# Performance work log

Measured on AMD Instinct MI355X. Metric: run time of the kernel, lower is better.

## Reference

```python
import jax, jax.numpy as jnp
import numpy as np

N, IN_FEAT, OUT_FEAT = 8192, 512, 256
SLOPE = 0.1


def setup_inputs() -> dict:
    key = jax.random.key(0)
    k1, k2, k3, k4, k5 = jax.random.split(key, 5)
    doc = jax.random.normal(k1, (N, IN_FEAT), dtype=jnp.float32)
    W = jax.random.normal(k2, (IN_FEAT, OUT_FEAT), dtype=jnp.float32) * (1.0 / np.sqrt(IN_FEAT))
    W_b = jax.random.normal(k3, (OUT_FEAT,), dtype=jnp.float32) * 0.01
    a = jax.random.normal(k4, (2 * OUT_FEAT,), dtype=jnp.float32) * (1.0 / np.sqrt(2 * OUT_FEAT))
    a_b = jax.random.normal(k5, (1,), dtype=jnp.float32) * 0.01
    return {"doc": doc, "W": W, "W_b": W_b, "a": a, "a_b": a_b}


def reference(doc, W, W_b, a, a_b):
    # h = W(doc): [N, outFeat]
    h = doc @ W + W_b
    d = h.shape[-1]
    # aParams(cat(h_i, h_j)) = a1.h_i + a2.h_j + b  (avoids the O(N^2*2d) concat)
    a1, a2 = a[:d], a[d:]
    score = (h @ a1)[:, None] + (h @ a2)[None, :] + a_b[0]  # [N, N]
    score = jax.nn.leaky_relu(score, SLOPE)
    # adj=None path -> all-ones mask, the where() is a no-op
    att = jax.nn.softmax(score, axis=1)  # normalize over neighbors j
    out = jax.nn.leaky_relu(att @ h, SLOPE)  # [N, outFeat]
    return out, att
```

## Files before the change

kernel.cpp:

```cpp
#include <hip/hip_runtime.h>
#include <hip/hip_bf16.h>


typedef __attribute__((ext_vector_type(4))) float f32x4;
typedef __attribute__((ext_vector_type(8))) short short8;
typedef __attribute__((ext_vector_type(4))) unsigned short ushort4v;

#define SLOPE 0.1f
#define NROW 8192
#define DDIM 256

__device__ __forceinline__ float lrelu(float x){ return fmaxf(x, SLOPE * x); }

__device__ __forceinline__ unsigned short f2bf(float f){
  union { float f; unsigned u; } v; v.f = f;
  unsigned r = (v.u + 0x7fffu + ((v.u >> 16) & 1u)) >> 16;
  return (unsigned short)r;
}
__device__ __forceinline__ float bf2f(unsigned short u){
  union { unsigned u; float f; } v; v.u = (unsigned)u << 16; return v.f;
}
__device__ __forceinline__ unsigned cvt_pk_bf16(float lo, float hi){
  unsigned r;
  asm("v_cvt_pk_bf16_f32 %0, %1, %2" : "=v"(r) : "v"(lo), "v"(hi));
  return r;
}

__global__ __launch_bounds__(256) void k_prep(
    const float* __restrict__ W,
    unsigned short* __restrict__ Wt_hi, unsigned short* __restrict__ Wt_lo)
{
  const int tid = blockIdx.x * 256 + threadIdx.x;
  const int c = tid >> 7, kq = tid & 127;
  ushort4v hi, lo;
#pragma unroll
  for (int j = 0; j < 4; ++j) {
    const float v = W[(size_t)(kq * 4 + j) * 256 + c];
    hi[j] = f2bf(v);
    lo[j] = f2bf(v - bf2f(hi[j]));
  }
  *reinterpret_cast<ushort4v*>(Wt_hi + (size_t)c * 512 + kq * 4) = hi;
  *reinterpret_cast<ushort4v*>(Wt_lo + (size_t)c * 512 + kq * 4) = lo;
}

__global__ __launch_bounds__(512, 2) void k_h(
    const float* __restrict__ doc, const unsigned short* __restrict__ Wt_hi,
    const unsigned short* __restrict__ Wt_lo, const float* __restrict__ Wb,
    const float* __restrict__ a,
    unsigned short* __restrict__ ht, float* __restrict__ s1,
    float* __restrict__ e2, float* __restrict__ e02)
{
  __shared__ __align__(16) short8 aH[2][2][64];
  __shared__ __align__(16) short8 aL[2][2][64];
  __shared__ float sred[8][2][32];

  const int t = threadIdx.x, w = t >> 6, l = t & 63;
  const int lr = l & 15, lg = l >> 4;
  const int rb = blockIdx.x * 32;
  const int cb = w * 32;

  f32x4 acc[2][2];
#pragma unroll
  for (int rt = 0; rt < 2; ++rt)
#pragma unroll
    for (int ct = 0; ct < 2; ++ct) acc[rt][ct] = (f32x4){0.f, 0.f, 0.f, 0.f};

  const float* docp = doc + (size_t)(rb + w * 16 + lr) * 512 + lg * 8;

  f32x4 v0, v1;
  auto loadDoc = [&](int k0) { if (w < 2) {
      v0 = *reinterpret_cast<const f32x4*>(docp + k0);
      v1 = *reinterpret_cast<const f32x4*>(docp + k0 + 4);
  }};
  auto writeStage = [&](int pb) { if (w < 2) {
      union { short8 v; unsigned short u[8]; } hi, lo;
#pragma unroll
      for (int q = 0; q < 4; ++q) {
        hi.u[q] = f2bf(v0[q]);     lo.u[q] = f2bf(v0[q] - bf2f(hi.u[q]));
        hi.u[4+q] = f2bf(v1[q]);   lo.u[4+q] = f2bf(v1[q] - bf2f(hi.u[4+q]));
      }
      aH[pb][w][l] = hi.v;
      aL[pb][w][l] = lo.v;
  }};

  loadDoc(0); writeStage(0); loadDoc(32);

  for (int n = 0; n < 16; ++n) {
    const int kk = n * 32;
    const int par = n & 1;

    asm volatile("s_waitcnt lgkmcnt(0)\n\ts_barrier" ::: "memory");

    const short8 ah0 = aH[par][0][l];
    const short8 ah1 = aH[par][1][l];
    const short8 al0 = aL[par][0][l];
    const short8 al1 = aL[par][1][l];

    short8 bh[2], bl[2];
#pragma unroll
    for (int ct = 0; ct < 2; ++ct) {
      const size_t off = (size_t)(cb + ct * 16 + lr) * 512 + kk + lg * 8;
      bh[ct] = *reinterpret_cast<const short8*>(Wt_hi + off);
      bl[ct] = *reinterpret_cast<const short8*>(Wt_lo + off);
    }

    if (n + 1 < 16) writeStage(par ^ 1);
    if (n + 2 < 16) loadDoc((n + 2) * 32);

#pragma unroll
    for (int ct = 0; ct < 2; ++ct) {
      acc[0][ct] = __builtin_amdgcn_mfma_f32_16x16x32_bf16(ah0, bh[ct], acc[0][ct], 0, 0, 0);
      acc[1][ct] = __builtin_amdgcn_mfma_f32_16x16x32_bf16(ah1, bh[ct], acc[1][ct], 0, 0, 0);
      acc[0][ct] = __builtin_amdgcn_mfma_f32_16x16x32_bf16(ah0, bl[ct], acc[0][ct], 0, 0, 0);
      acc[1][ct] = __builtin_amdgcn_mfma_f32_16x16x32_bf16(ah1, bl[ct], acc[1][ct], 0, 0, 0);
      acc[0][ct] = __builtin_amdgcn_mfma_f32_16x16x32_bf16(al0, bh[ct], acc[0][ct], 0, 0, 0);
      acc[1][ct] = __builtin_amdgcn_mfma_f32_16x16x32_bf16(al1, bh[ct], acc[1][ct], 0, 0, 0);
    }
  }

  float bias[2];
#pragma unroll
  for (int ct = 0; ct < 2; ++ct) bias[ct] = Wb[cb + ct * 16 + lr];
#pragma unroll
  for (int rt = 0; rt < 2; ++rt)
#pragma unroll
    for (int ct = 0; ct < 2; ++ct) {
#pragma unroll
      for (int q = 0; q < 4; ++q) acc[rt][ct][q] += bias[ct];
      ushort4v u;
#pragma unroll
      for (int q = 0; q < 4; ++q) u[q] = f2bf(acc[rt][ct][q]);
      *reinterpret_cast<ushort4v*>(
          ht + (size_t)(cb + ct * 16 + lr) * 8192 + rb + rt * 16 + lg * 4) = u;
    }

  float a1c[2], a2c[2];
#pragma unroll
  for (int ct = 0; ct < 2; ++ct) {
    a1c[ct] = a[cb + ct * 16 + lr];
    a2c[ct] = a[256 + cb + ct * 16 + lr];
  }
  float p1[2][4], p2[2][4];
#pragma unroll
  for (int rt = 0; rt < 2; ++rt)
#pragma unroll
    for (int q = 0; q < 4; ++q) {
      float x1 = 0.f, x2 = 0.f;
#pragma unroll
      for (int ct = 0; ct < 2; ++ct) {
        x1 = fmaf(acc[rt][ct][q], a1c[ct], x1);
        x2 = fmaf(acc[rt][ct][q], a2c[ct], x2);
      }
#pragma unroll
      for (int off = 1; off < 16; off <<= 1) {
        x1 += __shfl_xor(x1, off);
        x2 += __shfl_xor(x2, off);
      }
      p1[rt][q] = x1; p2[rt][q] = x2;
    }
  __syncthreads();
  if (lr == 0) {
#pragma unroll
    for (int rt = 0; rt < 2; ++rt)
#pragma unroll
      for (int q = 0; q < 4; ++q) {
        sred[w][0][rt * 16 + lg * 4 + q] = p1[rt][q];
        sred[w][1][rt * 16 + lg * 4 + q] = p2[rt][q];
      }
  }
  __syncthreads();
  if (t < 32) {
    float v1s = 0.f, v2s = 0.f;
#pragma unroll
    for (int ww = 0; ww < 8; ++ww) { v1s += sred[ww][0][t]; v2s += sred[ww][1][t]; }
    const int r = rb + t;
    s1[r] = v1s;
    e2[r] = __expf(v2s);
    e02[r] = __expf(SLOPE * v2s);
  }
}

__global__ __launch_bounds__(256) void k_z(
    const float* __restrict__ s1, const float* __restrict__ e2g,
    const float* __restrict__ e02g, const float* __restrict__ abp,
    float* __restrict__ rowinfo)
{
  __shared__ __align__(16) float es[8192];
  __shared__ __align__(16) float fs[8192];
  const int t = threadIdx.x;
  for (int i = t * 4; i < 8192; i += 1024) {
    *reinterpret_cast<f32x4*>(&es[i]) = *reinterpret_cast<const f32x4*>(e2g + i);
    *reinterpret_cast<f32x4*>(&fs[i]) = *reinterpret_cast<const f32x4*>(e02g + i);
  }
  __syncthreads();
  const int w = t >> 6, l = t & 63;
  const float ab = abp[0];
  const int rb = blockIdx.x * 16 + w * 4;
  float T[4], E1[4], E01[4];
#pragma unroll
  for (int rr = 0; rr < 4; ++rr) {
    const float s1a = s1[rb + rr] + ab;
    E1[rr] = __expf(s1a); E01[rr] = __expf(SLOPE * s1a); T[rr] = __expf(-s1a);
  }
  float zA[4] = {0.f,0.f,0.f,0.f}, zB[4] = {0.f,0.f,0.f,0.f};
  for (int i = l * 4; i < 8192; i += 256) {
    const f32x4 e = *reinterpret_cast<const f32x4*>(&es[i]);
    const f32x4 f = *reinterpret_cast<const f32x4*>(&fs[i]);
#pragma unroll
    for (int rr = 0; rr < 4; ++rr)
#pragma unroll
      for (int q = 0; q < 4; ++q) {
        const bool c = (e[q] >= T[rr]);
        zA[rr] += c ? e[q] : 0.f;
        zB[rr] += c ? 0.f : f[q];
      }
  }
#pragma unroll
  for (int rr = 0; rr < 4; ++rr) {
    float z = E1[rr] * zA[rr] + E01[rr] * zB[rr];
#pragma unroll
    for (int off = 32; off > 0; off >>= 1) z += __shfl_down(z, off);
    if (l == 0) {
      const float iz = 1.0f / z;
      f32x4 ri = (f32x4){E1[rr] * iz, E01[rr] * iz, T[rr], iz};
      *reinterpret_cast<f32x4*>(rowinfo + (size_t)(rb + rr) * 4) = ri;
    }
  }
}

__global__ __launch_bounds__(512, 4) void k_att(
    const float* __restrict__ rowinfo, const float* __restrict__ e2g,
    const float* __restrict__ e02g, const unsigned short* __restrict__ ht,
    float* __restrict__ att, float* __restrict__ part, int CHUNK)
{
  extern __shared__ __align__(16) char smem[];
  char* plsb  = smem;
  float* e2s  = reinterpret_cast<float*>(smem + 8192);
  float* e02s = e2s + CHUNK;

  const int t = threadIdx.x, w = t >> 6, l = t & 63;
  const int lr = l & 15, lg = l >> 4;
  const int kbase = blockIdx.x * CHUNK;
  const int rb = blockIdx.y * 64;

  for (int i = t * 4; i < CHUNK; i += 2048) {
    *reinterpret_cast<f32x4*>(e2s + i)  = *reinterpret_cast<const f32x4*>(e2g + kbase + i);
    *reinterpret_cast<f32x4*>(e02s + i) = *reinterpret_cast<const f32x4*>(e02g + kbase + i);
  }

  const int r = l >> 3, jc = l & 7;
  const int rowW = rb + w * 8 + r;
  const f32x4 ri = *reinterpret_cast<const f32x4*>(rowinfo + (size_t)rowW * 4);
  const float E1z = ri[0], E01z = ri[1], T = ri[2];
  float* attW = att + (size_t)rowW * 8192 + kbase + jc * 4;
  const int fragoff = (w >> 1) * 1024 + ((jc >> 1) * 16 + (w & 1) * 8 + r) * 16 + (jc & 1) * 8;

  __syncthreads();

  auto gen = [&](int kw, int pb) {
    const f32x4 eA = *reinterpret_cast<const f32x4*>(e2s + kw + jc * 4);
    const f32x4 fA = *reinterpret_cast<const f32x4*>(e02s + kw + jc * 4);
    f32x4 pA;
#pragma unroll
    for (int q = 0; q < 4; ++q) {
      const bool cA = (eA[q] >= T);
      pA[q] = (cA ? E1z : E01z) * (cA ? eA[q] : fA[q]);
    }
    *reinterpret_cast<f32x4*>(attW + kw) = pA;
    uint2 u;
    u.x = cvt_pk_bf16(pA[0], pA[1]); u.y = cvt_pk_bf16(pA[2], pA[3]);
    *reinterpret_cast<uint2*>(plsb + pb * 4096 + fragoff) = u;
  };

  const unsigned short* hbase = ht + (size_t)(w * 32 + lr) * 8192 + kbase + lg * 8;
  auto loadB = [&](short8* b, int n) {
    const int kk = n * 32;
    b[0] = *reinterpret_cast<const short8*>(hbase + kk);
    b[1] = *reinterpret_cast<const short8*>(hbase + kk + (size_t)16 * 8192);
  };

  f32x4 acc[4][2];
#pragma unroll
  for (int rt = 0; rt < 4; ++rt)
#pragma unroll
    for (int ct = 0; ct < 2; ++ct) acc[rt][ct] = (f32x4){0.f, 0.f, 0.f, 0.f};

  auto mma = [&](const short8* b, const short8& af0, const short8& af1,
                 const short8& af2, const short8& af3) {
    __builtin_amdgcn_s_setprio(1);
    acc[0][0] = __builtin_amdgcn_mfma_f32_16x16x32_bf16(af0, b[0], acc[0][0], 0, 0, 0);
    acc[1][0] = __builtin_amdgcn_mfma_f32_16x16x32_bf16(af1, b[0], acc[1][0], 0, 0, 0);
    acc[2][0] = __builtin_amdgcn_mfma_f32_16x16x32_bf16(af2, b[0], acc[2][0], 0, 0, 0);
    acc[3][0] = __builtin_amdgcn_mfma_f32_16x16x32_bf16(af3, b[0], acc[3][0], 0, 0, 0);
    acc[0][1] = __builtin_amdgcn_mfma_f32_16x16x32_bf16(af0, b[1], acc[0][1], 0, 0, 0);
    acc[1][1] = __builtin_amdgcn_mfma_f32_16x16x32_bf16(af1, b[1], acc[1][1], 0, 0, 0);
    acc[2][1] = __builtin_amdgcn_mfma_f32_16x16x32_bf16(af2, b[1], acc[2][1], 0, 0, 0);
    acc[3][1] = __builtin_amdgcn_mfma_f32_16x16x32_bf16(af3, b[1], acc[3][1], 0, 0, 0);
    __builtin_amdgcn_s_setprio(0);
  };

  short8 bAr[2], bBr[2];
  loadB(bAr, 0);
  gen(0, 0);

  const int NIT = CHUNK / 32;
  const short8* buf0 = reinterpret_cast<const short8*>(plsb);
  const short8* buf1 = reinterpret_cast<const short8*>(plsb + 4096);

  for (int n = 0; n < NIT; n += 2) {
    if (n + 1 < NIT) loadB(bBr, n + 1);
    asm volatile("s_waitcnt lgkmcnt(0)\n\ts_barrier" ::: "memory");
    {
      const short8 af0 = buf0[0 * 64 + l];
      const short8 af1 = buf0[1 * 64 + l];
      const short8 af2 = buf0[2 * 64 + l];
      const short8 af3 = buf0[3 * 64 + l];
      if (n + 1 < NIT) gen((n + 1) * 32, 1);
      mma(bAr, af0, af1, af2, af3);
    }
    if (n + 1 >= NIT) break;
    if (n + 2 < NIT) loadB(bAr, n + 2);
    asm volatile("s_waitcnt lgkmcnt(0)\n\ts_barrier" ::: "memory");
    {
      const short8 af0 = buf1[0 * 64 + l];
      const short8 af1 = buf1[1 * 64 + l];
      const short8 af2 = buf1[2 * 64 + l];
      const short8 af3 = buf1[3 * 64 + l];
      if (n + 2 < NIT) gen((n + 2) * 32, 0);
      mma(bBr, af0, af1, af2, af3);
    }
  }

  float* pb = part + (size_t)blockIdx.x * ((size_t)NROW * DDIM);
#pragma unroll
  for (int rt = 0; rt < 4; ++rt)
#pragma unroll
    for (int ct = 0; ct < 2; ++ct)
#pragma unroll
      for (int q = 0; q < 4; ++q)
        __builtin_nontemporal_store(acc[rt][ct][q],
            pb + (size_t)(rb + rt * 16 + lg * 4 + q) * 256 + w * 32 + ct * 16 + lr);
}

__global__ __launch_bounds__(256) void k_reduce(
    const float* __restrict__ part, float* __restrict__ out, int KS)
{
  const size_t idx = ((size_t)blockIdx.x * 256 + threadIdx.x) * 4;
  f32x4 s = __builtin_nontemporal_load(reinterpret_cast<const f32x4*>(part + idx));
  for (int k = 1; k < KS; ++k) {
    const f32x4 v = __builtin_nontemporal_load(
        reinterpret_cast<const f32x4*>(part + (size_t)k * NROW * DDIM + idx));
#pragma unroll
    for (int q = 0; q < 4; ++q) s[q] += v[q];
  }
#pragma unroll
  for (int q = 0; q < 4; ++q) s[q] = lrelu(s[q]);
  __builtin_nontemporal_store(s, reinterpret_cast<f32x4*>(out + idx));
}

extern "C" void kernel_launch(void* const* d_in, const int* in_sizes, int n_in,
                              void* d_out, int out_size, void* d_ws, size_t ws_size,
                              hipStream_t stream)
{
  const float* doc = (const float*)d_in[0];
  const float* W   = (const float*)d_in[1];
  const float* Wb  = (const float*)d_in[2];
  const float* a   = (const float*)d_in[3];
  const float* ab  = (const float*)d_in[4];

  float* out = (float*)d_out;
  float* att = out + (size_t)8192 * 256;

  char* ws = (char*)d_ws;
  unsigned short* ht    = (unsigned short*)ws;
  unsigned short* Wt_hi = (unsigned short*)(ws + (size_t)4 * 1024 * 1024);
  unsigned short* Wt_lo = Wt_hi + (size_t)256 * 512;
  float* s1      = (float*)(ws + (size_t)4 * 1024 * 1024 + 512 * 1024);
  float* e2      = s1 + 8192;
  float* e02     = e2 + 8192;
  float* rowinfo = e02 + 8192;
  const size_t base = (size_t)5 * 1024 * 1024;
  const size_t partBytes = (size_t)NROW * DDIM * sizeof(float);

  int KS = 1;
  for (int c = 4; c >= 1; c >>= 1)
    if (base + (size_t)c * partBytes <= ws_size) { KS = c; break; }
  float* part = (float*)(ws + base);
  const int CHUNK = NROW / KS;
  const size_t smem = 8192 + (size_t)2 * CHUNK * sizeof(float);

  hipLaunchKernelGGL(k_prep,   dim3(128),     dim3(256), 0,    stream, W, Wt_hi, Wt_lo);
  hipLaunchKernelGGL(k_h,      dim3(256),     dim3(512), 0,    stream, doc, Wt_hi, Wt_lo, Wb, a, ht, s1, e2, e02);
  hipLaunchKernelGGL(k_z,      dim3(512),     dim3(256), 0,    stream, s1, e2, e02, ab, rowinfo);
  hipLaunchKernelGGL(k_att,    dim3(KS, 128), dim3(512), smem, stream, rowinfo, e2, e02, ht, att, part, CHUNK);
  hipLaunchKernelGGL(k_reduce, dim3(2048),    dim3(256), 0,    stream, part, out, KS);
}
```

Measured before the change: 133.4 us.

## Fuse row normalization and reduction into single full-K attention kernel

Removes the separate k_z normalizer kernel and the split-K partial buffer plus k_reduce. Each block now owns 32 rows over the full 8192 columns, computes its row sums in-block from bf16 copies of e2/e02 held in LDS, and writes leaky-relu output directly. It also staggers each block's start column to spread ht reads, and uses nontemporal stores for att. The cost is 256 blocks instead of 512, so fewer waves are in flight, and the bf16 e-values used for both the normalizer and att values lose precision versus fp32.

```diff
diff --git a/kernel.cpp b/kernel.cpp
--- a/kernel.cpp
+++ b/kernel.cpp
@@ -180,182 +180,142 @@
   }
 }
 
-__global__ __launch_bounds__(256) void k_z(
-    const float* __restrict__ s1, const float* __restrict__ e2g,
-    const float* __restrict__ e02g, const float* __restrict__ abp,
-    float* __restrict__ rowinfo)
+__global__ __launch_bounds__(512, 2) void k_att(
+    const float* __restrict__ s1g, const float* __restrict__ abp,
+    const float* __restrict__ e2g, const float* __restrict__ e02g,
+    const unsigned short* __restrict__ ht,
+    float* __restrict__ att, float* __restrict__ out)
 {
-  __shared__ __align__(16) float es[8192];
-  __shared__ __align__(16) float fs[8192];
-  const int t = threadIdx.x;
-  for (int i = t * 4; i < 8192; i += 1024) {
-    *reinterpret_cast<f32x4*>(&es[i]) = *reinterpret_cast<const f32x4*>(e2g + i);
-    *reinterpret_cast<f32x4*>(&fs[i]) = *reinterpret_cast<const f32x4*>(e02g + i);
-  }
-  __syncthreads();
-  const int w = t >> 6, l = t & 63;
-  const float ab = abp[0];
-  const int rb = blockIdx.x * 16 + w * 4;
-  float T[4], E1[4], E01[4];
-#pragma unroll
-  for (int rr = 0; rr < 4; ++rr) {
-    const float s1a = s1[rb + rr] + ab;
-    E1[rr] = __expf(s1a); E01[rr] = __expf(SLOPE * s1a); T[rr] = __expf(-s1a);
-  }
-  float zA[4] = {0.f,0.f,0.f,0.f}, zB[4] = {0.f,0.f,0.f,0.f};
-  for (int i = l * 4; i < 8192; i += 256) {
-    const f32x4 e = *reinterpret_cast<const f32x4*>(&es[i]);
-    const f32x4 f = *reinterpret_cast<const f32x4*>(&fs[i]);
-#pragma unroll
-    for (int rr = 0; rr < 4; ++rr)
-#pragma unroll
-      for (int q = 0; q < 4; ++q) {
-        const bool c = (e[q] >= T[rr]);
-        zA[rr] += c ? e[q] : 0.f;
-        zB[rr] += c ? 0.f : f[q];
-      }
-  }
-#pragma unroll
-  for (int rr = 0; rr < 4; ++rr) {
-    float z = E1[rr] * zA[rr] + E01[rr] * zB[rr];
-#pragma unroll
-    for (int off = 32; off > 0; off >>= 1) z += __shfl_down(z, off);
-    if (l == 0) {
-      const float iz = 1.0f / z;
-      f32x4 ri = (f32x4){E1[rr] * iz, E01[rr] * iz, T[rr], iz};
-      *reinterpret_cast<f32x4*>(rowinfo + (size_t)(rb + rr) * 4) = ri;
-    }
-  }
-}
-
-__global__ __launch_bounds__(512, 4) void k_att(
-    const float* __restrict__ rowinfo, const float* __restrict__ e2g,
-    const float* __restrict__ e02g, const unsigned short* __restrict__ ht,
-    float* __restrict__ att, float* __restrict__ part, int CHUNK)
-{
-  extern __shared__ __align__(16) char smem[];
-  char* plsb  = smem;
-  float* e2s  = reinterpret_cast<float*>(smem + 8192);
-  float* e02s = e2s + CHUNK;
+  __shared__ __align__(16) unsigned short e2b[8192];
+  __shared__ __align__(16) unsigned short e02b[8192];
+  __shared__ __align__(16) short8 FR[2][4][2][64];
+  f32x4* rowinfoL = reinterpret_cast<f32x4*>(&FR[0][0][0][0]);
 
   const int t = threadIdx.x, w = t >> 6, l = t & 63;
   const int lr = l & 15, lg = l >> 4;
-  const int kbase = blockIdx.x * CHUNK;
-  const int rb = blockIdx.y * 64;
-
-  for (int i = t * 4; i < CHUNK; i += 2048) {
-    *reinterpret_cast<f32x4*>(e2s + i)  = *reinterpret_cast<const f32x4*>(e2g + kbase + i);
-    *reinterpret_cast<f32x4*>(e02s + i) = *reinterpret_cast<const f32x4*>(e02g + kbase + i);
-  }
-
-  const int r = l >> 3, jc = l & 7;
-  const int rowW = rb + w * 8 + r;
-  const f32x4 ri = *reinterpret_cast<const f32x4*>(rowinfo + (size_t)rowW * 4);
-  const float E1z = ri[0], E01z = ri[1], T = ri[2];
-  float* attW = att + (size_t)rowW * 8192 + kbase + jc * 4;
-  const int fragoff = (w >> 1) * 1024 + ((jc >> 1) * 16 + (w & 1) * 8 + r) * 16 + (jc & 1) * 8;
-
-  __syncthreads();
-
-  auto gen = [&](int kw, int pb) {
-    const f32x4 eA = *reinterpret_cast<const f32x4*>(e2s + kw + jc * 4);
-    const f32x4 fA = *reinterpret_cast<const f32x4*>(e02s + kw + jc * 4);
-    f32x4 pA;
-#pragma unroll
-    for (int q = 0; q < 4; ++q) {
-      const bool cA = (eA[q] >= T);
-      pA[q] = (cA ? E1z : E01z) * (cA ? eA[q] : fA[q]);
-    }
-    *reinterpret_cast<f32x4*>(attW + kw) = pA;
-    uint2 u;
-    u.x = cvt_pk_bf16(pA[0], pA[1]); u.y = cvt_pk_bf16(pA[2], pA[3]);
-    *reinterpret_cast<uint2*>(plsb + pb * 4096 + fragoff) = u;
+  const int rb = blockIdx.x * 32;
+
+  for (int i = t * 4; i < 8192; i += 2048) {
+    const f32x4 ev = *reinterpret_cast<const f32x4*>(e2g + i);
+    const f32x4 fv = *reinterpret_cast<const f32x4*>(e02g + i);
+    uint2 pe, pf;
+    pe.x = cvt_pk_bf16(ev[0], ev[1]); pe.y = cvt_pk_bf16(ev[2], ev[3]);
+    pf.x = cvt_pk_bf16(fv[0], fv[1]); pf.y = cvt_pk_bf16(fv[2], fv[3]);
+    *reinterpret_cast<uint2*>(&e2b[i])  = pe;
+    *reinterpret_cast<uint2*>(&e02b[i]) = pf;
+  }
+  __syncthreads();
+
+  {
+    const int zr = t >> 4, sub = t & 15;
+    const float s1a = s1g[rb + zr] + abp[0];
+    const float E1 = __expf(s1a), E01 = __expf(SLOPE * s1a), Tv = __expf(-s1a);
+    float zA = 0.f, zB = 0.f;
+    for (int jj = sub * 512; jj < sub * 512 + 512; jj += 8) {
+      const short8 eb = *reinterpret_cast<const short8*>(&e2b[jj]);
+      const short8 fb = *reinterpret_cast<const short8*>(&e02b[jj]);
+      union { short8 v; unsigned short u[8]; } eu, fu; eu.v = eb; fu.v = fb;
+#pragma unroll
+      for (int q = 0; q < 8; ++q) {
+        const float e = bf2f(eu.u[q]);
+        const bool c = (e >= Tv);
+        zA += c ? e : 0.f;
+        zB += c ? 0.f : bf2f(fu.u[q]);
+      }
+    }
+#pragma unroll
+    for (int off = 1; off < 16; off <<= 1) { zA += __shfl_xor(zA, off); zB += __shfl_xor(zB, off); }
+    if (sub == 0) {
+      const float z = E1 * zA + E01 * zB;
+      const float iz = 1.0f / z;
+      rowinfoL[zr] = (f32x4){E1 * iz, E01 * iz, Tv, iz};
+    }
+  }
+  __syncthreads();
+
+  const int wrt = w >> 2;
+  const int wrow = wrt * 16 + lr;
+  const f32x4 wri = rowinfoL[wrow];
+  const float E1z = wri[0], E01z = wri[1], T = wri[2];
+  float* attW = att + (size_t)(rb + wrow) * 8192 + lg * 8;
+  __syncthreads();
+
+  auto gen = [&](int q, int parw) {
+    const int win = q * 4 + (w & 3);
+    const int jb = win * 32 + lg * 8;
+    union { short8 v; unsigned short u[8]; } eu, fu;
+    eu.v = *reinterpret_cast<const short8*>(&e2b[jb]);
+    fu.v = *reinterpret_cast<const short8*>(&e02b[jb]);
+    f32x4 pA, pB;
+#pragma unroll
+    for (int qq = 0; qq < 4; ++qq) {
+      const float eA = bf2f(eu.u[qq]),     fA = bf2f(fu.u[qq]);
+      const float eB = bf2f(eu.u[4 + qq]), fB = bf2f(fu.u[4 + qq]);
+      const bool cA = (eA >= T);
+      pA[qq] = (cA ? E1z : E01z) * (cA ? eA : fA);
+      const bool cB = (eB >= T);
+      pB[qq] = (cB ? E1z : E01z) * (cB ? eB : fB);
+    }
+    __builtin_nontemporal_store(pA, reinterpret_cast<f32x4*>(attW + win * 32));
+    __builtin_nontemporal_store(pB, reinterpret_cast<f32x4*>(attW + win * 32 + 4));
+    union { short8 v; unsigned u[4]; } pk;
+    pk.u[0] = cvt_pk_bf16(pA[0], pA[1]); pk.u[1] = cvt_pk_bf16(pA[2], pA[3]);
+    pk.u[2] = cvt_pk_bf16(pB[0], pB[1]); pk.u[3] = cvt_pk_bf16(pB[2], pB[3]);
+    FR[parw][w & 3][wrt][l] = pk.v;
   };
 
-  const unsigned short* hbase = ht + (size_t)(w * 32 + lr) * 8192 + kbase + lg * 8;
-  auto loadB = [&](short8* b, int n) {
-    const int kk = n * 32;
+  const unsigned short* hbase = ht + (size_t)(w * 32 + lr) * 8192 + lg * 8;
+  auto loadB = [&](short8* b, int m) {
+    const int kk = m * 32;
     b[0] = *reinterpret_cast<const short8*>(hbase + kk);
     b[1] = *reinterpret_cast<const short8*>(hbase + kk + (size_t)16 * 8192);
   };
 
-  f32x4 acc[4][2];
-#pragma unroll
-  for (int rt = 0; rt < 4; ++rt)
-#pragma unroll
-    for (int ct = 0; ct < 2; ++ct) acc[rt][ct] = (f32x4){0.f, 0.f, 0.f, 0.f};
-
-  auto mma = [&](const short8* b, const short8& af0, const short8& af1,
-                 const short8& af2, const short8& af3) {
+  f32x4 acc00 = {0,0,0,0}, acc01 = {0,0,0,0}, acc10 = {0,0,0,0}, acc11 = {0,0,0,0};
+
+  auto mma = [&](const short8* b, int par, int u) {
+    const short8* fr = &FR[par][u][0][0];
+    const short8 af0 = fr[l];
+    const short8 af1 = fr[64 + l];
     __builtin_amdgcn_s_setprio(1);
-    acc[0][0] = __builtin_amdgcn_mfma_f32_16x16x32_bf16(af0, b[0], acc[0][0], 0, 0, 0);
-    acc[1][0] = __builtin_amdgcn_mfma_f32_16x16x32_bf16(af1, b[0], acc[1][0], 0, 0, 0);
-    acc[2][0] = __builtin_amdgcn_mfma_f32_16x16x32_bf16(af2, b[0], acc[2][0], 0, 0, 0);
-    acc[3][0] = __builtin_amdgcn_mfma_f32_16x16x32_bf16(af3, b[0], acc[3][0], 0, 0, 0);
-    acc[0][1] = __builtin_amdgcn_mfma_f32_16x16x32_bf16(af0, b[1], acc[0][1], 0, 0, 0);
-    acc[1][1] = __builtin_amdgcn_mfma_f32_16x16x32_bf16(af1, b[1], acc[1][1], 0, 0, 0);
-    acc[2][1] = __builtin_amdgcn_mfma_f32_16x16x32_bf16(af2, b[1], acc[2][1], 0, 0, 0);
-    acc[3][1] = __builtin_amdgcn_mfma_f32_16x16x32_bf16(af3, b[1], acc[3][1], 0, 0, 0);
+    acc00 = __builtin_amdgcn_mfma_f32_16x16x32_bf16(af0, b[0], acc00, 0, 0, 0);
+    acc10 = __builtin_amdgcn_mfma_f32_16x16x32_bf16(af1, b[0], acc10, 0, 0, 0);
+    acc01 = __builtin_amdgcn_mfma_f32_16x16x32_bf16(af0, b[1], acc01, 0, 0, 0);
+    acc11 = __builtin_amdgcn_mfma_f32_16x16x32_bf16(af1, b[1], acc11, 0, 0, 0);
     __builtin_amdgcn_s_setprio(0);
   };
 
+  const int ro = (blockIdx.x * 23) & 63;
+
   short8 bAr[2], bBr[2];
-  loadB(bAr, 0);
-  gen(0, 0);
-
-  const int NIT = CHUNK / 32;
-  const short8* buf0 = reinterpret_cast<const short8*>(plsb);
-  const short8* buf1 = reinterpret_cast<const short8*>(plsb + 4096);
-
-  for (int n = 0; n < NIT; n += 2) {
-    if (n + 1 < NIT) loadB(bBr, n + 1);
+  const int q0 = ro;
+  gen(q0, 0);
+  loadB(bAr, q0 * 4);
+
+  for (int p = 0; p < 64; ++p) {
+    const int q = (p + ro) & 63;
+    const int par = p & 1;
     asm volatile("s_waitcnt lgkmcnt(0)\n\ts_barrier" ::: "memory");
-    {
-      const short8 af0 = buf0[0 * 64 + l];
-      const short8 af1 = buf0[1 * 64 + l];
-      const short8 af2 = buf0[2 * 64 + l];
-      const short8 af3 = buf0[3 * 64 + l];
-      if (n + 1 < NIT) gen((n + 1) * 32, 1);
-      mma(bAr, af0, af1, af2, af3);
-    }
-    if (n + 1 >= NIT) break;
-    if (n + 2 < NIT) loadB(bAr, n + 2);
-    asm volatile("s_waitcnt lgkmcnt(0)\n\ts_barrier" ::: "memory");
-    {
-      const short8 af0 = buf1[0 * 64 + l];
-      const short8 af1 = buf1[1 * 64 + l];
-      const short8 af2 = buf1[2 * 64 + l];
-      const short8 af3 = buf1[3 * 64 + l];
-      if (n + 2 < NIT) gen((n + 2) * 32, 0);
-      mma(bBr, af0, af1, af2, af3);
-    }
-  }
-
-  float* pb = part + (size_t)blockIdx.x * ((size_t)NROW * DDIM);
-#pragma unroll
-  for (int rt = 0; rt < 4; ++rt)
-#pragma unroll
-    for (int ct = 0; ct < 2; ++ct)
-#pragma unroll
-      for (int q = 0; q < 4; ++q)
-        __builtin_nontemporal_store(acc[rt][ct][q],
-            pb + (size_t)(rb + rt * 16 + lg * 4 + q) * 256 + w * 32 + ct * 16 + lr);
-}
-
-__global__ __launch_bounds__(256) void k_reduce(
-    const float* __restrict__ part, float* __restrict__ out, int KS)
-{
-  const size_t idx = ((size_t)blockIdx.x * 256 + threadIdx.x) * 4;
-  f32x4 s = __builtin_nontemporal_load(reinterpret_cast<const f32x4*>(part + idx));
-  for (int k = 1; k < KS; ++k) {
-    const f32x4 v = __builtin_nontemporal_load(
-        reinterpret_cast<const f32x4*>(part + (size_t)k * NROW * DDIM + idx));
-#pragma unroll
-    for (int q = 0; q < 4; ++q) s[q] += v[q];
-  }
-#pragma unroll
-  for (int q = 0; q < 4; ++q) s[q] = lrelu(s[q]);
-  __builtin_nontemporal_store(s, reinterpret_cast<f32x4*>(out + idx));
+    if (p + 1 < 64) gen((p + 1 + ro) & 63, par ^ 1);
+    loadB(bBr, q * 4 + 1);
+    mma(bAr, par, 0);
+    loadB(bAr, q * 4 + 2);
+    mma(bBr, par, 1);
+    loadB(bBr, q * 4 + 3);
+    mma(bAr, par, 2);
+    if (p + 1 < 64) loadB(bAr, ((p + 1 + ro) & 63) * 4);
+    mma(bBr, par, 3);
+  }
+
+#pragma unroll
+  for (int q = 0; q < 4; ++q) {
+    const size_t r0 = (size_t)(rb + 0 * 16 + lg * 4 + q) * 256 + w * 32 + lr;
+    const size_t r1 = (size_t)(rb + 1 * 16 + lg * 4 + q) * 256 + w * 32 + lr;
+    __builtin_nontemporal_store(lrelu(acc00[q]), out + r0);
+    __builtin_nontemporal_store(lrelu(acc01[q]), out + r0 + 16);
+    __builtin_nontemporal_store(lrelu(acc10[q]), out + r1);
+    __builtin_nontemporal_store(lrelu(acc11[q]), out + r1 + 16);
+  }
 }
 
 extern "C" void kernel_launch(void* const* d_in, const int* in_sizes, int n_in,
@@ -375,23 +335,11 @@
   unsigned short* ht    = (unsigned short*)ws;
   unsigned short* Wt_hi = (unsigned short*)(ws + (size_t)4 * 1024 * 1024);
   unsigned short* Wt_lo = Wt_hi + (size_t)256 * 512;
-  float* s1      = (float*)(ws + (size_t)4 * 1024 * 1024 + 512 * 1024);
-  float* e2      = s1 + 8192;
-  float* e02     = e2 + 8192;
-  float* rowinfo = e02 + 8192;
-  const size_t base = (size_t)5 * 1024 * 1024;
-  const size_t partBytes = (size_t)NROW * DDIM * sizeof(float);
-
-  int KS = 1;
-  for (int c = 4; c >= 1; c >>= 1)
-    if (base + (size_t)c * partBytes <= ws_size) { KS = c; break; }
-  float* part = (float*)(ws + base);
-  const int CHUNK = NROW / KS;
-  const size_t smem = 8192 + (size_t)2 * CHUNK * sizeof(float);
-
-  hipLaunchKernelGGL(k_prep,   dim3(128),     dim3(256), 0,    stream, W, Wt_hi, Wt_lo);
-  hipLaunchKernelGGL(k_h,      dim3(256),     dim3(512), 0,    stream, doc, Wt_hi, Wt_lo, Wb, a, ht, s1, e2, e02);
-  hipLaunchKernelGGL(k_z,      dim3(512),     dim3(256), 0,    stream, s1, e2, e02, ab, rowinfo);
-  hipLaunchKernelGGL(k_att,    dim3(KS, 128), dim3(512), smem, stream, rowinfo, e2, e02, ht, att, part, CHUNK);
-  hipLaunchKernelGGL(k_reduce, dim3(2048),    dim3(256), 0,    stream, part, out, KS);
-}
+  float* s1  = (float*)(ws + (size_t)4 * 1024 * 1024 + 512 * 1024);
+  float* e2  = s1 + 8192;
+  float* e02 = e2 + 8192;
+
+  hipLaunchKernelGGL(k_prep, dim3(128), dim3(256), 0, stream, W, Wt_hi, Wt_lo);
+  hipLaunchKernelGGL(k_h,    dim3(256), dim3(512), 0, stream, doc, Wt_hi, Wt_lo, Wb, a, ht, s1, e2, e02);
+  hipLaunchKernelGGL(k_att,  dim3(256), dim3(512), 0, stream, s1, ab, e2, e02, ht, att, out);
+}
```

Result: slower. 201.2 us (+50.9%).
